# Optimization experiments

Measured on AMD Instinct MI355X. Metric: run time of the kernel, lower is better.

Reference implementation:

```python
import jax, jax.numpy as jnp
import numpy as np

S = 1048576   # sequence length (only free scale knob)
D = 20        # d_model (forced == d_internal by the original code)
DI = 20       # d_internal (forced to 20 by output_i[:20])
C = 3         # num_classes
L = 2         # num_layers


def setup_inputs() -> dict:
    key = jax.random.key(0)
    ks = jax.random.split(key, 13)
    f = lambda k, shp, s=1.0: jax.random.normal(k, shp, dtype=jnp.float32) * s
    return {
        "indices": f(ks[0], (S, D)),
        # per-layer stacked parameters (leading axis L)
        "Wq":   f(ks[1], (L, DI, D)),          # torch.randn(d_internal, d)
        "Wk":   f(ks[2], (L, DI, D)),
        "Wv":   f(ks[3], (L, D, D)),           # torch.randn(d, d)
        "Wres": f(ks[4], (L, D, DI)),          # W_residual: (d, d_internal)
        "W1":   f(ks[5], (L, D, DI), 0.2),     # Linear(d_internal, d_model).weight
        "b1":   f(ks[6], (L, D), 0.2),
        "W2":   f(ks[7], (L, D, DI), 0.2),     # second Linear(d_internal, d_model)
        "b2":   f(ks[8], (L, D), 0.2),
        "W3":   f(ks[9], (L, D, D), 0.2),      # Linear(input_dim=d, d_model) residual proj
        "b3":   f(ks[10], (L, D), 0.2),
        "Wc":   f(ks[11], (C, D), 0.2),        # final Linear(d_model, num_classes)
        "bc":   f(ks[12], (C,), 0.2),
    }


def _layer(x, Wq, Wk, Wv, Wres, W1, b1, W2, b2, W3, b3):
    # Vectorized form of the original per-token Python loop.
    q = x @ Wq.T                                   # (S, DI)
    k = x @ Wk.T                                   # (S, DI)
    v = x @ Wv.T                                   # (S, D)
    # scalar similarity per token; softmax over a singleton axis == 1.0 (kept for fidelity)
    sim = jnp.sum(q * k, axis=-1, keepdims=True) / np.sqrt(DI)   # (S, 1)
    p = jax.nn.softmax(sim, axis=-1)               # all ones
    out = (p * v)[:, :DI]                          # output_i = v_i[:20]
    out = out + x @ Wres                           # residual via W_residual
    out = jax.nn.relu(out @ W1.T + b1)             # linear1 + relu
    out = out @ W2.T + b2                          # linear2
    out = out + x @ W3.T + b3                      # final input residual projection
    return out


def reference(indices, Wq, Wk, Wv, Wres, W1, b1, W2, b2, W3, b3, Wc, bc):
    x = indices
    for l in range(L):  # small fixed layer count
        x = _layer(x, Wq[l], Wk[l], Wv[l], Wres[l], W1[l], b1[l], W2[l], b2[l], W3[l], b3[l])
    logits = x @ Wc.T + bc                         # (S, C)
    return jax.nn.softmax(logits, axis=1)
```

## Files before the change

kernel.cpp:

```cpp
#include <hip/hip_runtime.h>
#include <math.h>


#define OFF_G1   0
#define OFF_P1   400
#define OFF_P2   800
#define OFF_M2   1200
#define OFF_Q1   1260
#define OFF_Q2   1320
#define OFF_B11  1380
#define OFF_F2   1400
#define OFF_F3   1420
#define NWTOT    1423

__global__ void prep_kernel(const float* __restrict__ Wv, const float* __restrict__ Wres,
                            const float* __restrict__ W1, const float* __restrict__ b1,
                            const float* __restrict__ W2, const float* __restrict__ b2,
                            const float* __restrict__ W3, const float* __restrict__ b3,
                            const float* __restrict__ Wc, const float* __restrict__ bc,
                            float* __restrict__ W) {
    __shared__ float G2[400];
    __shared__ float M3[60];
    __shared__ float e1[20];
    const int tid = threadIdx.x;
    for (int idx = tid; idx < 480; idx += 256) {
        if (idx < 400) {
            const int i = idx / 20, m = idx % 20;
            float s = 0.f;
            for (int j = 0; j < 20; ++j)
                s = fmaf(Wv[400 + j*20 + i] + Wres[400 + i*20 + j], W1[400 + m*20 + j], s);
            G2[idx] = s;
        } else if (idx < 460) {
            const int r = idx - 400, i = r / 3, c = r % 3;
            float s = 0.f;
            for (int p = 0; p < 20; ++p)
                s = fmaf(Wc[c*20 + p], W3[400 + p*20 + i], s);
            M3[r] = s;
        } else {
            const int j = idx - 460;
            e1[j] = b2[j] + b3[j];
        }
    }
    __syncthreads();
    for (int idx = tid; idx < NWTOT; idx += 256) {
        float s = 0.f;
        if (idx < 400) {
            const int k = idx / 20, m = idx % 20;
            for (int j = 0; j < 20; ++j)
                s = fmaf(Wv[j*20 + k] + Wres[k*20 + j], W1[m*20 + j], s);
        } else if (idx < 800) {
            const int r = idx - 400, mp = r / 20, m = r % 20;
            for (int i = 0; i < 20; ++i)
                s = fmaf(W2[i*20 + mp], G2[i*20 + m], s);
        } else if (idx < 1200) {
            const int r = idx - 800, k = r / 20, m = r % 20;
            for (int i = 0; i < 20; ++i)
                s = fmaf(W3[i*20 + k], G2[i*20 + m], s);
        } else if (idx < 1260) {
            const int r = idx - 1200, c = r / 20, m = r % 20;
            for (int p = 0; p < 20; ++p)
                s = fmaf(Wc[c*20 + p], W2[400 + p*20 + m], s);
        } else if (idx < 1320) {
            const int r = idx - 1260, c = r / 20, mp = r % 20;
            for (int i = 0; i < 20; ++i)
                s = fmaf(W2[i*20 + mp], M3[i*3 + c], s);
        } else if (idx < 1380) {
            const int r = idx - 1320, c = r / 20, k = r % 20;
            for (int i = 0; i < 20; ++i)
                s = fmaf(W3[i*20 + k], M3[i*3 + c], s);
        } else if (idx < 1400) {
            s = b1[idx - 1380];
        } else if (idx < 1420) {
            const int m = idx - 1400;
            s = b1[20 + m];
            for (int i = 0; i < 20; ++i)
                s = fmaf(e1[i], G2[i*20 + m], s);
        } else {
            const int c = idx - 1420;
            s = bc[c];
            for (int p = 0; p < 20; ++p)
                s = fmaf(Wc[c*20 + p], b2[20 + p] + b3[20 + p], s);
            for (int i = 0; i < 20; ++i)
                s = fmaf(e1[i], M3[i*3 + c], s);
        }
        W[idx] = s;
    }
}

typedef float v4f __attribute__((ext_vector_type(4)));
typedef const __attribute__((address_space(4))) v4f  c4f_t;
typedef const __attribute__((address_space(4))) float cfl_t;

__global__ __launch_bounds__(256, 6) void fwd_kernel(const float* __restrict__ X,
                                                     const float* __restrict__ Wg,
                                                     float* __restrict__ out, int ntok) {
    c4f_t* W4 = (c4f_t*)(unsigned long long)Wg;
    cfl_t* Wf = (cfl_t*)(unsigned long long)Wg;

    const int tid = blockIdx.x * blockDim.x + threadIdx.x;
    if (tid >= ntok) return;

    float x[20];
    const float4* xp = reinterpret_cast<const float4*>(X + (size_t)tid * 20);
    #pragma unroll
    for (int q = 0; q < 5; ++q) {
        const float4 v = xp[q];
        x[4*q+0] = v.x; x[4*q+1] = v.y; x[4*q+2] = v.z; x[4*q+3] = v.w;
    }

    float la[3];
    #pragma unroll
    for (int c = 0; c < 3; ++c) {
        float s = Wf[OFF_F3 + c];
        #pragma unroll
        for (int q = 0; q < 5; ++q) {
            const v4f w = W4[OFF_Q2/4 + c*5 + q];
            s = fmaf(x[4*q+0], w.x, s);
            s = fmaf(x[4*q+1], w.y, s);
            s = fmaf(x[4*q+2], w.z, s);
            s = fmaf(x[4*q+3], w.w, s);
        }
        la[c] = s;
    }

    float h[20];
    #pragma unroll
    for (int q = 0; q < 5; ++q) {
        const v4f b = W4[OFF_B11/4 + q];
        h[4*q+0] = b.x; h[4*q+1] = b.y; h[4*q+2] = b.z; h[4*q+3] = b.w;
    }
    #pragma unroll
    for (int k = 0; k < 20; ++k) {
        const float x0 = x[k];
        #pragma unroll
        for (int q = 0; q < 5; ++q) {
            const v4f w = W4[OFF_G1/4 + k*5 + q];
            h[4*q+0] = fmaf(x0, w.x, h[4*q+0]);
            h[4*q+1] = fmaf(x0, w.y, h[4*q+1]);
            h[4*q+2] = fmaf(x0, w.z, h[4*q+2]);
            h[4*q+3] = fmaf(x0, w.w, h[4*q+3]);
        }
    }
    #pragma unroll
    for (int i = 0; i < 20; ++i) h[i] = fmaxf(h[i], 0.f);

    #pragma unroll
    for (int c = 0; c < 3; ++c) {
        float s = la[c];
        #pragma unroll
        for (int q = 0; q < 5; ++q) {
            const v4f w = W4[OFF_Q1/4 + c*5 + q];
            s = fmaf(h[4*q+0], w.x, s);
            s = fmaf(h[4*q+1], w.y, s);
            s = fmaf(h[4*q+2], w.z, s);
            s = fmaf(h[4*q+3], w.w, s);
        }
        la[c] = s;
    }

    float g[20];
    #pragma unroll
    for (int q = 0; q < 5; ++q) {
        const v4f b = W4[OFF_F2/4 + q];
        g[4*q+0] = b.x; g[4*q+1] = b.y; g[4*q+2] = b.z; g[4*q+3] = b.w;
    }
    #pragma unroll
    for (int k = 0; k < 20; ++k) {
        const float h0 = h[k];
        #pragma unroll
        for (int q = 0; q < 5; ++q) {
            const v4f w = W4[OFF_P1/4 + k*5 + q];
            g[4*q+0] = fmaf(h0, w.x, g[4*q+0]);
            g[4*q+1] = fmaf(h0, w.y, g[4*q+1]);
            g[4*q+2] = fmaf(h0, w.z, g[4*q+2]);
            g[4*q+3] = fmaf(h0, w.w, g[4*q+3]);
        }
        const float x0 = x[k];
        #pragma unroll
        for (int q = 0; q < 5; ++q) {
            const v4f w = W4[OFF_P2/4 + k*5 + q];
            g[4*q+0] = fmaf(x0, w.x, g[4*q+0]);
            g[4*q+1] = fmaf(x0, w.y, g[4*q+1]);
            g[4*q+2] = fmaf(x0, w.z, g[4*q+2]);
            g[4*q+3] = fmaf(x0, w.w, g[4*q+3]);
        }
    }
    #pragma unroll
    for (int i = 0; i < 20; ++i) g[i] = fmaxf(g[i], 0.f);

    #pragma unroll
    for (int c = 0; c < 3; ++c) {
        float s = la[c];
        #pragma unroll
        for (int q = 0; q < 5; ++q) {
            const v4f w = W4[OFF_M2/4 + c*5 + q];
            s = fmaf(g[4*q+0], w.x, s);
            s = fmaf(g[4*q+1], w.y, s);
            s = fmaf(g[4*q+2], w.z, s);
            s = fmaf(g[4*q+3], w.w, s);
        }
        la[c] = s;
    }

    const float m = fmaxf(fmaxf(la[0], la[1]), la[2]);
    const float e0 = __expf(la[0] - m), e1 = __expf(la[1] - m), e2 = __expf(la[2] - m);
    const float r = 1.f / (e0 + e1 + e2);
    float* o = out + (size_t)tid * 3;
    o[0] = e0 * r;
    o[1] = e1 * r;
    o[2] = e2 * r;
}

extern "C" void kernel_launch(void* const* d_in, const int* in_sizes, int n_in,
                              void* d_out, int out_size, void* d_ws, size_t ws_size,
                              hipStream_t stream) {
    const float* X    = (const float*)d_in[0];
    const float* Wv   = (const float*)d_in[3];
    const float* Wres = (const float*)d_in[4];
    const float* W1   = (const float*)d_in[5];
    const float* b1   = (const float*)d_in[6];
    const float* W2   = (const float*)d_in[7];
    const float* b2   = (const float*)d_in[8];
    const float* W3   = (const float*)d_in[9];
    const float* b3   = (const float*)d_in[10];
    const float* Wc   = (const float*)d_in[11];
    const float* bc   = (const float*)d_in[12];
    float* out = (float*)d_out;
    float* W   = (float*)d_ws;

    const int S = in_sizes[0] / 20;

    prep_kernel<<<1, 256, 0, stream>>>(Wv, Wres, W1, b1, W2, b2, W3, b3, Wc, bc, W);

    const int block = 256;
    const int grid = (S + block - 1) / block;
    fwd_kernel<<<grid, block, 0, stream>>>(X, W, out, S);
}
```

Baseline: 172.4 us.

## Process four tokens per thread with weights staged in shared memory

Each thread now handles four tokens, so every weight vector read is reused across four tokens. The folded weights are copied into LDS per block instead of read through scalar constant loads. Small classifier matrices are transposed and padded to float4 rows, and the three outputs per token are written as packed float4 stores. The cost is much higher register pressure (launch bounds drop to 2 blocks per CU), fewer waves to hide memory latency, and an assumption that the token count is a multiple of four.

```diff
diff --git a/kernel.cpp b/kernel.cpp
--- a/kernel.cpp
+++ b/kernel.cpp
@@ -5,13 +5,13 @@
 #define OFF_G1   0
 #define OFF_P1   400
 #define OFF_P2   800
-#define OFF_M2   1200
-#define OFF_Q1   1260
-#define OFF_Q2   1320
-#define OFF_B11  1380
-#define OFF_F2   1400
-#define OFF_F3   1420
-#define NWTOT    1423
+#define OFF_M2T  1200
+#define OFF_Q1T  1280
+#define OFF_Q2T  1360
+#define OFF_B11  1440
+#define OFF_F2   1460
+#define OFF_F3   1480
+#define NWTOT    1484
 
 __global__ void prep_kernel(const float* __restrict__ Wv, const float* __restrict__ Wres,
                             const float* __restrict__ W1, const float* __restrict__ b1,
@@ -56,159 +56,174 @@
             const int r = idx - 800, k = r / 20, m = r % 20;
             for (int i = 0; i < 20; ++i)
                 s = fmaf(W3[i*20 + k], G2[i*20 + m], s);
-        } else if (idx < 1260) {
-            const int r = idx - 1200, c = r / 20, m = r % 20;
-            for (int p = 0; p < 20; ++p)
-                s = fmaf(Wc[c*20 + p], W2[400 + p*20 + m], s);
-        } else if (idx < 1320) {
-            const int r = idx - 1260, c = r / 20, mp = r % 20;
-            for (int i = 0; i < 20; ++i)
-                s = fmaf(W2[i*20 + mp], M3[i*3 + c], s);
-        } else if (idx < 1380) {
-            const int r = idx - 1320, c = r / 20, k = r % 20;
-            for (int i = 0; i < 20; ++i)
-                s = fmaf(W3[i*20 + k], M3[i*3 + c], s);
-        } else if (idx < 1400) {
-            s = b1[idx - 1380];
-        } else if (idx < 1420) {
-            const int m = idx - 1400;
+        } else if (idx < 1280) {
+            const int r = idx - 1200, m = r / 4, c = r % 4;
+            if (c < 3)
+                for (int p = 0; p < 20; ++p)
+                    s = fmaf(Wc[c*20 + p], W2[400 + p*20 + m], s);
+        } else if (idx < 1360) {
+            const int r = idx - 1280, k = r / 4, c = r % 4;
+            if (c < 3)
+                for (int i = 0; i < 20; ++i)
+                    s = fmaf(W2[i*20 + k], M3[i*3 + c], s);
+        } else if (idx < 1440) {
+            const int r = idx - 1360, k = r / 4, c = r % 4;
+            if (c < 3)
+                for (int i = 0; i < 20; ++i)
+                    s = fmaf(W3[i*20 + k], M3[i*3 + c], s);
+        } else if (idx < 1460) {
+            s = b1[idx - 1440];
+        } else if (idx < 1480) {
+            const int m = idx - 1460;
             s = b1[20 + m];
             for (int i = 0; i < 20; ++i)
                 s = fmaf(e1[i], G2[i*20 + m], s);
         } else {
-            const int c = idx - 1420;
-            s = bc[c];
-            for (int p = 0; p < 20; ++p)
-                s = fmaf(Wc[c*20 + p], b2[20 + p] + b3[20 + p], s);
-            for (int i = 0; i < 20; ++i)
-                s = fmaf(e1[i], M3[i*3 + c], s);
+            const int c = idx - 1480;
+            if (c < 3) {
+                s = bc[c];
+                for (int p = 0; p < 20; ++p)
+                    s = fmaf(Wc[c*20 + p], b2[20 + p] + b3[20 + p], s);
+                for (int i = 0; i < 20; ++i)
+                    s = fmaf(e1[i], M3[i*3 + c], s);
+            }
         }
         W[idx] = s;
     }
 }
 
 typedef float v4f __attribute__((ext_vector_type(4)));
-typedef const __attribute__((address_space(4))) v4f  c4f_t;
-typedef const __attribute__((address_space(4))) float cfl_t;
-
-__global__ __launch_bounds__(256, 6) void fwd_kernel(const float* __restrict__ X,
+
+__global__ __launch_bounds__(256, 2) void fwd_kernel(const float* __restrict__ X,
                                                      const float* __restrict__ Wg,
                                                      float* __restrict__ out, int ntok) {
-    c4f_t* W4 = (c4f_t*)(unsigned long long)Wg;
-    cfl_t* Wf = (cfl_t*)(unsigned long long)Wg;
-
-    const int tid = blockIdx.x * blockDim.x + threadIdx.x;
-    if (tid >= ntok) return;
-
-    float x[20];
-    const float4* xp = reinterpret_cast<const float4*>(X + (size_t)tid * 20);
-    #pragma unroll
-    for (int q = 0; q < 5; ++q) {
-        const float4 v = xp[q];
-        x[4*q+0] = v.x; x[4*q+1] = v.y; x[4*q+2] = v.z; x[4*q+3] = v.w;
-    }
-
-    float la[3];
-    #pragma unroll
-    for (int c = 0; c < 3; ++c) {
-        float s = Wf[OFF_F3 + c];
-        #pragma unroll
-        for (int q = 0; q < 5; ++q) {
-            const v4f w = W4[OFF_Q2/4 + c*5 + q];
-            s = fmaf(x[4*q+0], w.x, s);
-            s = fmaf(x[4*q+1], w.y, s);
-            s = fmaf(x[4*q+2], w.z, s);
-            s = fmaf(x[4*q+3], w.w, s);
-        }
-        la[c] = s;
-    }
-
-    float h[20];
+    __shared__ float Ws[NWTOT];
+    for (int i = threadIdx.x; i < NWTOT; i += 256) Ws[i] = Wg[i];
+    __syncthreads();
+    const v4f* W4 = reinterpret_cast<const v4f*>(Ws);
+
+    const int t0 = (blockIdx.x * 256 + threadIdx.x) * 4;
+    if (t0 >= ntok) return;
+    const float4* xp = reinterpret_cast<const float4*>(X + (size_t)t0 * 20);
+
+    float h[4][20], g[4][20], la[4][3];
+
     #pragma unroll
     for (int q = 0; q < 5; ++q) {
         const v4f b = W4[OFF_B11/4 + q];
-        h[4*q+0] = b.x; h[4*q+1] = b.y; h[4*q+2] = b.z; h[4*q+3] = b.w;
-    }
+        const v4f f = W4[OFF_F2/4 + q];
+        #pragma unroll
+        for (int j = 0; j < 4; ++j) {
+            h[j][4*q+0] = b.x; h[j][4*q+1] = b.y; h[j][4*q+2] = b.z; h[j][4*q+3] = b.w;
+            g[j][4*q+0] = f.x; g[j][4*q+1] = f.y; g[j][4*q+2] = f.z; g[j][4*q+3] = f.w;
+        }
+    }
+    {
+        const v4f f3v = W4[OFF_F3/4];
+        #pragma unroll
+        for (int j = 0; j < 4; ++j) { la[j][0] = f3v.x; la[j][1] = f3v.y; la[j][2] = f3v.z; }
+    }
+
+    #pragma unroll 1
+    for (int q = 0; q < 5; ++q) {
+        float xc[4][4];
+        #pragma unroll
+        for (int j = 0; j < 4; ++j) {
+            const float4 v = xp[j*5 + q];
+            xc[j][0] = v.x; xc[j][1] = v.y; xc[j][2] = v.z; xc[j][3] = v.w;
+        }
+        #pragma unroll
+        for (int d = 0; d < 4; ++d) {
+            const int k = 4*q + d;
+            const v4f wq2 = W4[OFF_Q2T/4 + k];
+            #pragma unroll
+            for (int j = 0; j < 4; ++j) {
+                la[j][0] = fmaf(xc[j][d], wq2.x, la[j][0]);
+                la[j][1] = fmaf(xc[j][d], wq2.y, la[j][1]);
+                la[j][2] = fmaf(xc[j][d], wq2.z, la[j][2]);
+            }
+            #pragma unroll
+            for (int r = 0; r < 5; ++r) {
+                const v4f wg = W4[OFF_G1/4 + k*5 + r];
+                #pragma unroll
+                for (int j = 0; j < 4; ++j) {
+                    h[j][4*r+0] = fmaf(xc[j][d], wg.x, h[j][4*r+0]);
+                    h[j][4*r+1] = fmaf(xc[j][d], wg.y, h[j][4*r+1]);
+                    h[j][4*r+2] = fmaf(xc[j][d], wg.z, h[j][4*r+2]);
+                    h[j][4*r+3] = fmaf(xc[j][d], wg.w, h[j][4*r+3]);
+                }
+            }
+            #pragma unroll
+            for (int r = 0; r < 5; ++r) {
+                const v4f wp = W4[OFF_P2/4 + k*5 + r];
+                #pragma unroll
+                for (int j = 0; j < 4; ++j) {
+                    g[j][4*r+0] = fmaf(xc[j][d], wp.x, g[j][4*r+0]);
+                    g[j][4*r+1] = fmaf(xc[j][d], wp.y, g[j][4*r+1]);
+                    g[j][4*r+2] = fmaf(xc[j][d], wp.z, g[j][4*r+2]);
+                    g[j][4*r+3] = fmaf(xc[j][d], wp.w, g[j][4*r+3]);
+                }
+            }
+        }
+    }
+
+    #pragma unroll
+    for (int j = 0; j < 4; ++j)
+        #pragma unroll
+        for (int i = 0; i < 20; ++i) h[j][i] = fmaxf(h[j][i], 0.f);
+
     #pragma unroll
     for (int k = 0; k < 20; ++k) {
-        const float x0 = x[k];
-        #pragma unroll
-        for (int q = 0; q < 5; ++q) {
-            const v4f w = W4[OFF_G1/4 + k*5 + q];
-            h[4*q+0] = fmaf(x0, w.x, h[4*q+0]);
-            h[4*q+1] = fmaf(x0, w.y, h[4*q+1]);
-            h[4*q+2] = fmaf(x0, w.z, h[4*q+2]);
-            h[4*q+3] = fmaf(x0, w.w, h[4*q+3]);
-        }
-    }
-    #pragma unroll
-    for (int i = 0; i < 20; ++i) h[i] = fmaxf(h[i], 0.f);
-
-    #pragma unroll
-    for (int c = 0; c < 3; ++c) {
-        float s = la[c];
-        #pragma unroll
-        for (int q = 0; q < 5; ++q) {
-            const v4f w = W4[OFF_Q1/4 + c*5 + q];
-            s = fmaf(h[4*q+0], w.x, s);
-            s = fmaf(h[4*q+1], w.y, s);
-            s = fmaf(h[4*q+2], w.z, s);
-            s = fmaf(h[4*q+3], w.w, s);
-        }
-        la[c] = s;
-    }
-
-    float g[20];
-    #pragma unroll
-    for (int q = 0; q < 5; ++q) {
-        const v4f b = W4[OFF_F2/4 + q];
-        g[4*q+0] = b.x; g[4*q+1] = b.y; g[4*q+2] = b.z; g[4*q+3] = b.w;
-    }
+        const v4f wq1 = W4[OFF_Q1T/4 + k];
+        #pragma unroll
+        for (int j = 0; j < 4; ++j) {
+            la[j][0] = fmaf(h[j][k], wq1.x, la[j][0]);
+            la[j][1] = fmaf(h[j][k], wq1.y, la[j][1]);
+            la[j][2] = fmaf(h[j][k], wq1.z, la[j][2]);
+        }
+        #pragma unroll
+        for (int r = 0; r < 5; ++r) {
+            const v4f wp = W4[OFF_P1/4 + k*5 + r];
+            #pragma unroll
+            for (int j = 0; j < 4; ++j) {
+                g[j][4*r+0] = fmaf(h[j][k], wp.x, g[j][4*r+0]);
+                g[j][4*r+1] = fmaf(h[j][k], wp.y, g[j][4*r+1]);
+                g[j][4*r+2] = fmaf(h[j][k], wp.z, g[j][4*r+2]);
+                g[j][4*r+3] = fmaf(h[j][k], wp.w, g[j][4*r+3]);
+            }
+        }
+    }
+
+    #pragma unroll
+    for (int j = 0; j < 4; ++j)
+        #pragma unroll
+        for (int i = 0; i < 20; ++i) g[j][i] = fmaxf(g[j][i], 0.f);
+
     #pragma unroll
     for (int k = 0; k < 20; ++k) {
-        const float h0 = h[k];
-        #pragma unroll
-        for (int q = 0; q < 5; ++q) {
-            const v4f w = W4[OFF_P1/4 + k*5 + q];
-            g[4*q+0] = fmaf(h0, w.x, g[4*q+0]);
-            g[4*q+1] = fmaf(h0, w.y, g[4*q+1]);
-            g[4*q+2] = fmaf(h0, w.z, g[4*q+2]);
-            g[4*q+3] = fmaf(h0, w.w, g[4*q+3]);
-        }
-        const float x0 = x[k];
-        #pragma unroll
-        for (int q = 0; q < 5; ++q) {
-            const v4f w = W4[OFF_P2/4 + k*5 + q];
-            g[4*q+0] = fmaf(x0, w.x, g[4*q+0]);
-            g[4*q+1] = fmaf(x0, w.y, g[4*q+1]);
-            g[4*q+2] = fmaf(x0, w.z, g[4*q+2]);
-            g[4*q+3] = fmaf(x0, w.w, g[4*q+3]);
-        }
-    }
-    #pragma unroll
-    for (int i = 0; i < 20; ++i) g[i] = fmaxf(g[i], 0.f);
-
-    #pragma unroll
-    for (int c = 0; c < 3; ++c) {
-        float s = la[c];
-        #pragma unroll
-        for (int q = 0; q < 5; ++q) {
-            const v4f w = W4[OFF_M2/4 + c*5 + q];
-            s = fmaf(g[4*q+0], w.x, s);
-            s = fmaf(g[4*q+1], w.y, s);
-            s = fmaf(g[4*q+2], w.z, s);
-            s = fmaf(g[4*q+3], w.w, s);
-        }
-        la[c] = s;
-    }
-
-    const float m = fmaxf(fmaxf(la[0], la[1]), la[2]);
-    const float e0 = __expf(la[0] - m), e1 = __expf(la[1] - m), e2 = __expf(la[2] - m);
-    const float r = 1.f / (e0 + e1 + e2);
-    float* o = out + (size_t)tid * 3;
-    o[0] = e0 * r;
-    o[1] = e1 * r;
-    o[2] = e2 * r;
+        const v4f wm = W4[OFF_M2T/4 + k];
+        #pragma unroll
+        for (int j = 0; j < 4; ++j) {
+            la[j][0] = fmaf(g[j][k], wm.x, la[j][0]);
+            la[j][1] = fmaf(g[j][k], wm.y, la[j][1]);
+            la[j][2] = fmaf(g[j][k], wm.z, la[j][2]);
+        }
+    }
+
+    float p[12];
+    #pragma unroll
+    for (int j = 0; j < 4; ++j) {
+        const float m = fmaxf(fmaxf(la[j][0], la[j][1]), la[j][2]);
+        const float e0 = __expf(la[j][0] - m);
+        const float e1 = __expf(la[j][1] - m);
+        const float e2 = __expf(la[j][2] - m);
+        const float r = 1.f / (e0 + e1 + e2);
+        p[3*j+0] = e0 * r; p[3*j+1] = e1 * r; p[3*j+2] = e2 * r;
+    }
+    float4* op = reinterpret_cast<float4*>(out + (size_t)t0 * 3);
+    op[0] = make_float4(p[0], p[1], p[2], p[3]);
+    op[1] = make_float4(p[4], p[5], p[6], p[7]);
+    op[2] = make_float4(p[8], p[9], p[10], p[11]);
 }
 
 extern "C" void kernel_launch(void* const* d_in, const int* in_sizes, int n_in,
@@ -232,7 +247,8 @@
 
     prep_kernel<<<1, 256, 0, stream>>>(Wv, Wres, W1, b1, W2, b2, W3, b3, Wc, bc, W);
 
+    const int nthreads = S / 4;
     const int block = 256;
-    const int grid = (S + block - 1) / block;
+    const int grid = (nthreads + block - 1) / block;
     fwd_kernel<<<grid, block, 0, stream>>>(X, W, out, S);
 }
```

New measurement: 259.5 us. +50.5%, slower.
